# Kernel tuning notes

Measured on AMD Instinct MI355X. Metric: run time of the kernel, lower is better.

## Reference

```python
import math
import jax, jax.numpy as jnp
import numpy as np

B, L, HID = 2, 2048, 2048
H = 16
D = HID // H  # 128
EPS = 1e-6
ROPE_BASE = 10000.0
BETA_MIN, BETA_MAX = 0.8, 0.9995


def _rope_cache(seq_len, dim):
    half = dim // 2
    inv_freq = 1.0 / (ROPE_BASE ** (jnp.arange(half, dtype=jnp.float32) / float(half)))
    t = jnp.arange(seq_len, dtype=jnp.float32)
    freqs = t[:, None] * inv_freq[None, :]  # [L, half]
    return jnp.cos(freqs), jnp.sin(freqs)


def _apply_rope(x, cos, sin):
    # x: [B, H, L, D]; cos/sin: [L, D//2]
    half = x.shape[-1] // 2
    xe, xo = x[..., :half], x[..., half:]
    c = cos[None, None]
    s = sin[None, None]
    return jnp.concatenate([xe * c - xo * s, xe * s + xo * c], axis=-1)


def setup_inputs() -> dict:
    key = jax.random.key(0)
    ks = jax.random.split(key, 6)
    sc = 1.0 / math.sqrt(HID)  # ~ xavier scale
    return {
        "x": jax.random.normal(ks[0], (B, L, HID), jnp.float32),
        "Wq": jax.random.normal(ks[1], (HID, HID), jnp.float32) * sc,
        "Wk": jax.random.normal(ks[2], (HID, HID), jnp.float32) * sc,
        "Wv": jax.random.normal(ks[3], (HID, HID), jnp.float32) * sc,
        "Wg": jax.random.normal(ks[4], (HID, H), jnp.float32) * sc,
        "bg": jnp.full((H,), math.log(0.98 / (1.0 - 0.98)), jnp.float32),
        "Wo": jax.random.normal(ks[5], (HID, HID), jnp.float32) * sc,
        "bo": jnp.zeros((HID,), jnp.float32),
    }


def _deltanet(x, Wq, Wk, Wv, Wg, bg, Wo, bo):
    Bb, Ll, _ = x.shape
    split = lambda t: t.reshape(Bb, Ll, H, D).transpose(0, 2, 1, 3)  # [B,H,L,D]
    q = split(x @ Wq)
    k = split(x @ Wk)
    v = split(x @ Wv)

    cos, sin = _rope_cache(Ll, D)
    q = _apply_rope(q, cos, sin)
    k = _apply_rope(k, cos, sin)

    beta = jax.nn.sigmoid(x @ Wg + bg)                # [B,L,H]
    beta = jnp.clip(beta, BETA_MIN, BETA_MAX).transpose(0, 2, 1)  # [B,H,L]

    phi_q = jax.nn.elu(q) + 1.0
    phi_k = jax.nn.elu(k) + 1.0

    # time-major for scan
    pq = phi_q.transpose(2, 0, 1, 3)  # [L,B,H,D]
    pk = phi_k.transpose(2, 0, 1, 3)
    vt = v.transpose(2, 0, 1, 3)
    bt = beta.transpose(2, 0, 1)      # [L,B,H]

    S0 = jnp.zeros((Bb, H, D, D), jnp.float32)
    z0 = jnp.zeros((Bb, H, D), jnp.float32)

    def step(carry, inp):
        S, z = carry
        pq_t, pk_t, v_t, b_t = inp
        S = S * b_t[..., None, None] + pk_t[..., :, None] * v_t[..., None, :]
        z = z * b_t[..., None] + pk_t
        numer = jnp.einsum('bhd,bhde->bhe', pq_t, S)
        denom = jnp.sum(pq_t * z, axis=-1, keepdims=True) + EPS
        return (S, z), numer / denom

    (_, _), y = jax.lax.scan(step, (S0, z0), (pq, pk, vt, bt))  # y: [L,B,H,D]
    y = y.transpose(1, 0, 2, 3).reshape(Bb, Ll, HID)  # [B,L,H*D]
    return y @ Wo + bo


def reference(x, Wq, Wk, Wv, Wg, bg, Wo, bo):
    return _deltanet(x, Wq, Wk, Wv, Wg, bg, Wo, bo)
```

## Files before the change

kernel.cpp:

```cpp
#include <hip/hip_runtime.h>


typedef __attribute__((ext_vector_type(8))) short short8;
typedef __attribute__((ext_vector_type(4))) float f32x4;

__device__ __forceinline__ unsigned short f2bf(float f) {
  unsigned u = __float_as_uint(f);
  u += 0x7fffu + ((u >> 16) & 1u);
  return (unsigned short)(u >> 16);
}
__device__ __forceinline__ float bf2f(unsigned short s) {
  return __uint_as_float(((unsigned)s) << 16);
}
__device__ __forceinline__ float phi_elu1(float x) {
  return x > 0.f ? x + 1.f : expf(x);
}
__device__ __forceinline__ void gl_lds16(const void* g, void* l) {
  __builtin_amdgcn_global_load_lds(
      (const __attribute__((address_space(1))) void*)g,
      (__attribute__((address_space(3))) void*)l, 16, 0, 0);
}
__device__ __forceinline__ void bar_raw() {
  asm volatile("" ::: "memory");
  __builtin_amdgcn_s_barrier();
  asm volatile("" ::: "memory");
}

__global__ __launch_bounds__(256)
void k_cast(const float* __restrict__ x, unsigned short* __restrict__ xb) {
  int i = (blockIdx.x * 256 + threadIdx.x) * 4;
  float4 f = *(const float4*)(x + i);
  uint2 p;
  p.x = (unsigned)f2bf(f.x) | ((unsigned)f2bf(f.y) << 16);
  p.y = (unsigned)f2bf(f.z) | ((unsigned)f2bf(f.w) << 16);
  *(uint2*)(xb + i) = p;
}

__global__ __launch_bounds__(256)
void k_transw(const float* __restrict__ Wq, const float* __restrict__ Wk,
              const float* __restrict__ Wv, const float* __restrict__ Wo,
              const float* __restrict__ Wg,
              unsigned short* __restrict__ Wt, unsigned short* __restrict__ Wot,
              unsigned short* __restrict__ Wgt16) {
  const int z = blockIdx.z;
  if (z == 4) {
    if (blockIdx.y != 0) return;
    int idx = blockIdx.x * 256 + threadIdx.x;
    int h = idx >> 9, k4 = (idx & 511) * 4;
    uint2 p;
    p.x = (unsigned)f2bf(Wg[(k4 + 0) * 16 + h]) | ((unsigned)f2bf(Wg[(k4 + 1) * 16 + h]) << 16);
    p.y = (unsigned)f2bf(Wg[(k4 + 2) * 16 + h]) | ((unsigned)f2bf(Wg[(k4 + 3) * 16 + h]) << 16);
    *(uint2*)(Wgt16 + (size_t)h * 2048 + k4) = p;
    return;
  }
  const float* W = (z == 0) ? Wq : (z == 1) ? Wk : (z == 2) ? Wv : Wo;
  unsigned short* out = (z < 3) ? (Wt + (size_t)z * 2048 * 2048) : Wot;
  __shared__ float tile[64][65];
  const int n0 = blockIdx.x * 64;
  const int k0 = blockIdx.y * 64;
  const int tx = threadIdx.x & 63;
  const int ty = threadIdx.x >> 6;
#pragma unroll
  for (int rl = 0; rl < 16; ++rl) {
    int kk = rl * 4 + ty;
    tile[kk][tx] = W[(size_t)(k0 + kk) * 2048 + n0 + tx];
  }
  __syncthreads();
#pragma unroll
  for (int rl = 0; rl < 16; ++rl) {
    int nn = rl * 4 + ty;
    out[(size_t)(n0 + nn) * 2048 + k0 + tx] = f2bf(tile[tx][nn]);
  }
}

__global__ __launch_bounds__(256)
void k_betaW(const unsigned short* __restrict__ xb, const unsigned short* __restrict__ Wgt16,
             const float* __restrict__ bg, float* __restrict__ beta) {
  const int w = threadIdx.x >> 6;
  const int lane = threadIdx.x & 63;
  const int m = blockIdx.x * 4 + w;
  const int h = lane & 15, kq = lane >> 4;
  const unsigned short* xr = xb + (size_t)m * 2048 + kq * 512;
  const unsigned short* wr = Wgt16 + (size_t)h * 2048 + kq * 512;
  float acc = 0.f;
#pragma unroll 8
  for (int i = 0; i < 64; ++i) {
    short8 xv = *(const short8*)(xr + i * 8);
    short8 wv = *(const short8*)(wr + i * 8);
#pragma unroll
    for (int j = 0; j < 8; ++j)
      acc = fmaf(bf2f((unsigned short)xv[j]), bf2f((unsigned short)wv[j]), acc);
  }
  acc += __shfl_xor(acc, 16, 64);
  acc += __shfl_xor(acc, 32, 64);
  if (lane < 16) {
    float v = acc + bg[h];
    float bv = 1.f / (1.f + expf(-v));
    beta[(size_t)m * 16 + h] = fminf(fmaxf(bv, 0.8f), 0.9995f);
  }
}

template <bool OUT_BF16, bool ADD_BIAS>
__global__ __launch_bounds__(256)
void k_gemm(const unsigned short* __restrict__ A, const unsigned short* __restrict__ Bt,
            void* __restrict__ Cptr, const float* __restrict__ bias,
            int M, int N, int K, int ldA, int ldC) {
  __shared__ __align__(16) unsigned short As[128][64];
  __shared__ __align__(16) unsigned short Bs[128][64];
  const int tid = threadIdx.x;
  const int n0 = blockIdx.x * 128;
  const int m0 = blockIdx.y * 128;
  const int lane = tid & 63;
  const int w = tid >> 6;
  const int wm = w >> 1, wn = w & 1;
  const int q = lane >> 4, r = lane & 15;

  const int srow0 = w * 8 + (lane >> 3);
  const int scol = ((lane & 7) ^ ((lane >> 3) & 7)) * 8;

  f32x4 acc[4][4];
#pragma unroll
  for (int i = 0; i < 4; ++i)
#pragma unroll
    for (int j = 0; j < 4; ++j) acc[i][j] = (f32x4){0.f, 0.f, 0.f, 0.f};

  const unsigned short* A0 = A + (size_t)(m0 + srow0) * ldA + scol;
  const unsigned short* B0 = Bt + (size_t)(n0 + srow0) * K + scol;
  unsigned short* lA = &As[srow0][(lane & 7) * 8];
  unsigned short* lB = &Bs[srow0][(lane & 7) * 8];

  const int rsw = r & 7;

  for (int kt = 0; kt < K; kt += 64) {
    __syncthreads();
#pragma unroll
    for (int i = 0; i < 4; ++i) {
      gl_lds16(A0 + (size_t)i * 32 * ldA + kt, lA + i * 2048);
      gl_lds16(B0 + (size_t)i * 32 * K + kt, lB + i * 2048);
    }
    __syncthreads();
#pragma unroll
    for (int kk = 0; kk < 2; ++kk) {
      const int ps = ((kk * 4 + q) ^ rsw) * 8;
      short8 af[4], bfr[4];
#pragma unroll
      for (int i = 0; i < 4; ++i)
        af[i] = *(const short8*)&As[wm * 64 + i * 16 + r][ps];
#pragma unroll
      for (int j = 0; j < 4; ++j)
        bfr[j] = *(const short8*)&Bs[wn * 64 + j * 16 + r][ps];
#pragma unroll
      for (int i = 0; i < 4; ++i)
#pragma unroll
        for (int j = 0; j < 4; ++j)
          acc[i][j] = __builtin_amdgcn_mfma_f32_16x16x32_bf16(af[i], bfr[j], acc[i][j], 0, 0, 0);
    }
  }
#pragma unroll
  for (int i = 0; i < 4; ++i) {
#pragma unroll
    for (int j = 0; j < 4; ++j) {
#pragma unroll
      for (int rr = 0; rr < 4; ++rr) {
        int mi = m0 + wm * 64 + i * 16 + q * 4 + rr;
        int ni = n0 + wn * 64 + j * 16 + r;
        float val = acc[i][j][rr];
        if (ADD_BIAS) val += bias[ni];
        if (OUT_BF16)
          ((unsigned short*)Cptr)[(size_t)mi * ldC + ni] = f2bf(val);
        else
          ((float*)Cptr)[(size_t)mi * ldC + ni] = val;
      }
    }
  }
}

template <bool OUT_BF16, bool ADD_BIAS>
__global__ __launch_bounds__(512, 2)
void k_gemm2(const unsigned short* __restrict__ A, const unsigned short* __restrict__ Bt,
             void* __restrict__ Cptr, const float* __restrict__ bias,
             int M, int N, int K, int ldA, int ldC) {
  __shared__ __align__(16) unsigned short Ls[3][3][128][64];
  const int tid = threadIdx.x;
  const int lane = tid & 63;
  const int w = tid >> 6;
  const int wm = w >> 1;
  const int wn = w & 1;
  const int ql = lane >> 4;
  const int r = lane & 15;

  const int nwg = gridDim.x * gridDim.y;
  const int orig = blockIdx.y * gridDim.x + blockIdx.x;
  const int li = (orig & 7) * (nwg >> 3) + (orig >> 3);
  const int m0 = (li & 15) * 256;
  const int n0 = (li >> 4) * 128;

  const int srow = tid >> 3;
  const int sphys = tid & 7;
  const int slog = sphys ^ (srow & 7);
  const unsigned short* Ab = A + (size_t)(m0 + srow) * ldA + slog * 8;
  const unsigned short* Bb = Bt + (size_t)(n0 + srow) * K + slog * 8;

#define STG(st, h, tt)                                                        \
  do {                                                                        \
    const size_t ldx = ((h) == 2) ? (size_t)K : (size_t)ldA;                  \
    const unsigned short* gs =                                                \
        (((h) == 2) ? Bb : (Ab + (size_t)((h) * 128) * ldA)) +                \
        (size_t)(tt) * 64;                                                    \
    unsigned short* ld = &Ls[(st)][(h)][srow][sphys * 8];                     \
    gl_lds16(gs, ld);                                                         \
    gl_lds16(gs + 64 * ldx, ld + 64 * 64);                                    \
  } while (0)

  f32x4 acc[4][4];
#pragma unroll
  for (int i = 0; i < 4; ++i)
#pragma unroll
    for (int j = 0; j < 4; ++j) acc[i][j] = (f32x4){0.f, 0.f, 0.f, 0.f};

  const int NT = K >> 6;

#pragma unroll
  for (int h = 0; h < 3; ++h) STG(0, h, 0);
#pragma unroll
  for (int h = 0; h < 3; ++h) STG(1, h, 1);
  asm volatile("s_waitcnt vmcnt(6)" ::: "memory");
  bar_raw();

  short8 bfr[4][2];

  for (int t = 0; t < NT; ++t) {
    const int st = t % 3;
    const unsigned short (*LA)[64] = Ls[st][wm >> 1];
    const unsigned short (*LB)[64] = Ls[st][2];
    const int arow0 = (wm & 1) * 64;
    const int brow0 = wn * 64;
    const bool pf = (t + 2 < NT);
    const int s2 = (t + 2) % 3;
#pragma unroll
    for (int p = 0; p < 2; ++p) {
      if (p == 0) {
#pragma unroll
        for (int nj = 0; nj < 4; ++nj)
#pragma unroll
          for (int kk = 0; kk < 2; ++kk)
            bfr[nj][kk] = *(const short8*)
                &LB[brow0 + nj * 16 + r][((kk * 4 + ql) ^ (r & 7)) * 8];
      }
      short8 af[2][2];
#pragma unroll
      for (int im = 0; im < 2; ++im)
#pragma unroll
        for (int kk = 0; kk < 2; ++kk)
          af[im][kk] = *(const short8*)
              &LA[arow0 + (p * 2 + im) * 16 + r][((kk * 4 + ql) ^ (r & 7)) * 8];
      if (pf) {
        if (p == 0) {
          STG(s2, 0, t + 2);
          STG(s2, 1, t + 2);
        } else {
          STG(s2, 2, t + 2);
        }
      }
      bar_raw();
      __builtin_amdgcn_s_setprio(1);
#pragma unroll
      for (int kk = 0; kk < 2; ++kk)
#pragma unroll
        for (int im = 0; im < 2; ++im)
#pragma unroll
          for (int nj = 0; nj < 4; ++nj)
            acc[p * 2 + im][nj] = __builtin_amdgcn_mfma_f32_16x16x32_bf16(
                af[im][kk], bfr[nj][kk], acc[p * 2 + im][nj], 0, 0, 0);
      __builtin_amdgcn_s_setprio(0);
      if (p == 1) {
        if (pf)
          asm volatile("s_waitcnt vmcnt(6)" ::: "memory");
        else if (t + 1 < NT)
          asm volatile("s_waitcnt vmcnt(0)" ::: "memory");
      }
      __builtin_amdgcn_sched_barrier(0);
      bar_raw();
    }
  }
#undef STG

#pragma unroll
  for (int mi = 0; mi < 4; ++mi) {
#pragma unroll
    for (int nj = 0; nj < 4; ++nj) {
#pragma unroll
      for (int rr = 0; rr < 4; ++rr) {
        int mrow = m0 + wm * 64 + mi * 16 + ql * 4 + rr;
        int ncol = n0 + wn * 64 + nj * 16 + r;
        float val = acc[mi][nj][rr];
        if (ADD_BIAS) val += bias[ncol];
        if (OUT_BF16)
          ((unsigned short*)Cptr)[(size_t)mrow * ldC + ncol] = f2bf(val);
        else
          ((float*)Cptr)[(size_t)mrow * ldC + ncol] = val;
      }
    }
  }
}

__global__ __launch_bounds__(256)
void k_prep(const unsigned short* __restrict__ qkv, const float* __restrict__ beta,
            unsigned short* __restrict__ Qt, unsigned short* __restrict__ Ktg,
            unsigned short* __restrict__ Ag, unsigned short* __restrict__ Vg,
            float* __restrict__ gch) {
  const int ch = blockIdx.x;
  const int bh = blockIdx.y;
  const int b = bh >> 4, h = bh & 15;
  const int tid = threadIdx.x;
  const int t0 = ch * 64;

  __shared__ float Gs[64];
  __shared__ unsigned short Qs[64][136];
  __shared__ unsigned short Ks[64][136];
  __shared__ unsigned short Vs[128][72];

  if (tid < 64) {
    float bb = beta[((size_t)(b * 2048 + t0 + tid)) * 16 + h];
#pragma unroll
    for (int off = 1; off < 64; off <<= 1) {
      float o = __shfl_up(bb, off, 64);
      if (tid >= off) bb *= o;
    }
    Gs[tid] = bb;
    if (tid == 63) gch[bh * 32 + ch] = bb;
  }
  __syncthreads();

  const int dgl = tid & 7;
  float invf[8];
#pragma unroll
  for (int j = 0; j < 8; ++j)
    invf[j] = expf((float)(dgl * 8 + j) * -0.14391156831212787f);

  int s = tid >> 3;
#pragma unroll
  for (int rep = 0; rep < 2; ++rep, s += 32) {
    size_t row = ((size_t)(b * 2048 + t0 + s)) * 6144 + (size_t)h * 128;
    short8 qlo = *(const short8*)(qkv + row + dgl * 8);
    short8 qhi = *(const short8*)(qkv + row + 64 + dgl * 8);
    short8 klo = *(const short8*)(qkv + row + 2048 + dgl * 8);
    short8 khi = *(const short8*)(qkv + row + 2048 + 64 + dgl * 8);
    float g = Gs[s];
    float ig = 1.f / g;
    float tg = (float)(t0 + s);
    short8 oql, oqh, okl, okh;
#pragma unroll
    for (int j = 0; j < 8; ++j) {
      float sn, cs;
      __sincosf(tg * invf[j], &sn, &cs);
      float qe = bf2f((unsigned short)qlo[j]), qo = bf2f((unsigned short)qhi[j]);
      float a0 = qe * cs - qo * sn, a1 = qe * sn + qo * cs;
      oql[j] = (short)f2bf(phi_elu1(a0) * g);
      oqh[j] = (short)f2bf(phi_elu1(a1) * g);
      float ke = bf2f((unsigned short)klo[j]), ko = bf2f((unsigned short)khi[j]);
      a0 = ke * cs - ko * sn;
      a1 = ke * sn + ko * cs;
      okl[j] = (short)f2bf(phi_elu1(a0) * ig);
      okh[j] = (short)f2bf(phi_elu1(a1) * ig);
    }
    size_t qbase = (((size_t)bh * 32 + ch) * 64 + s) * 128;
    *(short8*)(Qt + qbase + dgl * 8) = oql;
    *(short8*)(Qt + qbase + 64 + dgl * 8) = oqh;
    *(short8*)&Qs[s][dgl * 8] = oql;
    *(short8*)&Qs[s][64 + dgl * 8] = oqh;
    *(short8*)&Ks[s][dgl * 8] = okl;
    *(short8*)&Ks[s][64 + dgl * 8] = okh;
  }
  {
    const int s2 = tid >> 2, qe = tid & 3;
    const unsigned short* vrow =
        qkv + ((size_t)(b * 2048 + t0 + s2)) * 6144 + 4096 + (size_t)h * 128 + qe * 32;
#pragma unroll
    for (int i = 0; i < 4; ++i) {
      short8 vv = *(const short8*)(vrow + i * 8);
#pragma unroll
      for (int j = 0; j < 8; ++j) Vs[qe * 32 + i * 8 + j][s2] = (unsigned short)vv[j];
    }
  }
  __syncthreads();

  {
    const int d = tid >> 1, sh = tid & 1;
    unsigned pk[16];
#pragma unroll
    for (int i = 0; i < 16; ++i)
      pk[i] = (unsigned)Ks[sh * 32 + 2 * i][d] | ((unsigned)Ks[sh * 32 + 2 * i + 1][d] << 16);
    unsigned short* kr = Ktg + ((size_t)bh * 32 + ch) * 8192 + (size_t)d * 64 + sh * 32;
#pragma unroll
    for (int i = 0; i < 4; ++i)
      *(uint4*)(kr + i * 8) = *(uint4*)&pk[i * 4];
    unsigned short* vr = Vg + ((size_t)bh * 32 + ch) * 8192 + (size_t)d * 64 + sh * 32;
#pragma unroll
    for (int i = 0; i < 4; ++i)
      *(uint4*)(vr + i * 8) = *(const uint4*)&Vs[d][sh * 32 + i * 8];
  }

  {
    const int lane = tid & 63;
    const int w = tid >> 6;
    const int q = lane >> 4, r = lane & 15;
    f32x4 acc[4];
#pragma unroll
    for (int nt = 0; nt < 4; ++nt) acc[nt] = (f32x4){0.f, 0.f, 0.f, 0.f};
#pragma unroll
    for (int kk = 0; kk < 4; ++kk) {
      short8 af = *(const short8*)&Qs[w * 16 + r][kk * 32 + q * 8];
#pragma unroll
      for (int nt = 0; nt < 4; ++nt) {
        short8 bf = *(const short8*)&Ks[nt * 16 + r][kk * 32 + q * 8];
        acc[nt] = __builtin_amdgcn_mfma_f32_16x16x32_bf16(af, bf, acc[nt], 0, 0, 0);
      }
    }
    unsigned short* Agp = Ag + ((size_t)bh * 32 + ch) * 4096;
#pragma unroll
    for (int nt = 0; nt < 4; ++nt) {
#pragma unroll
      for (int rr = 0; rr < 4; ++rr) {
        int t_l = w * 16 + q * 4 + rr;
        int s_l = nt * 16 + r;
        float val = (s_l <= t_l) ? acc[nt][rr] : 0.f;
        Agp[t_l * 64 + s_l] = f2bf(val);
      }
    }
  }
}

__global__ __launch_bounds__(256)
void k_kv(const unsigned short* __restrict__ Ktg, const unsigned short* __restrict__ Vg,
          unsigned short* __restrict__ Mg, float* __restrict__ mzg) {
  const int ch = blockIdx.x, bh = blockIdx.y;
  const int tid = threadIdx.x, lane = tid & 63, w = tid >> 6;
  const int q = lane >> 4, r = lane & 15;
  __shared__ unsigned short Kts[128][72];
  __shared__ unsigned short Vs[128][72];
  const unsigned short* Kp = Ktg + ((size_t)bh * 32 + ch) * 8192;
  const unsigned short* Vp = Vg + ((size_t)bh * 32 + ch) * 8192;
#pragma unroll
  for (int i = 0; i < 4; ++i) {
    int c = tid + i * 256;
    int dd = c >> 3, sg = c & 7;
    *(int4*)&Kts[dd][sg * 8] = *(const int4*)(Kp + dd * 64 + sg * 8);
    *(int4*)&Vs[dd][sg * 8] = *(const int4*)(Vp + dd * 64 + sg * 8);
  }
  __syncthreads();
  f32x4 acc[2][8];
#pragma unroll
  for (int jj = 0; jj < 2; ++jj)
#pragma unroll
    for (int i = 0; i < 8; ++i) acc[jj][i] = (f32x4){0.f, 0.f, 0.f, 0.f};
#pragma unroll
  for (int kk = 0; kk < 2; ++kk) {
    short8 af[2];
    af[0] = *(const short8*)&Vs[(w * 2 + 0) * 16 + r][kk * 32 + q * 8];
    af[1] = *(const short8*)&Vs[(w * 2 + 1) * 16 + r][kk * 32 + q * 8];
#pragma unroll
    for (int i = 0; i < 8; ++i) {
      short8 bf = *(const short8*)&Kts[i * 16 + r][kk * 32 + q * 8];
      acc[0][i] = __builtin_amdgcn_mfma_f32_16x16x32_bf16(af[0], bf, acc[0][i], 0, 0, 0);
      acc[1][i] = __builtin_amdgcn_mfma_f32_16x16x32_bf16(af[1], bf, acc[1][i], 0, 0, 0);
    }
  }
  {
    int dd = tid >> 1, sh = tid & 1;
    const unsigned short* kp = &Kts[dd][sh * 32];
    float zs = 0.f;
#pragma unroll
    for (int i = 0; i < 4; ++i) {
      short8 kv = *(const short8*)(kp + i * 8);
#pragma unroll
      for (int j = 0; j < 8; ++j) zs += bf2f((unsigned short)kv[j]);
    }
    zs += __shfl_xor(zs, 1, 64);
    if (sh == 0) mzg[((size_t)bh * 32 + ch) * 128 + dd] = zs;
  }
  unsigned short* Mp = Mg + ((size_t)bh * 32 + ch) * 16384;
#pragma unroll
  for (int jj = 0; jj < 2; ++jj)
#pragma unroll
    for (int i = 0; i < 8; ++i)
#pragma unroll
      for (int rr = 0; rr < 4; ++rr) {
        int e = (w * 2 + jj) * 16 + q * 4 + rr;
        Mp[e * 128 + i * 16 + r] = f2bf(acc[jj][i][rr]);
      }
}

__global__ __launch_bounds__(256)
void k_sprefix(unsigned short* __restrict__ Msg, float* __restrict__ mzg,
               const float* __restrict__ gch) {
  const int es = blockIdx.x;
  const int bh = blockIdx.y;
  const int tid = threadIdx.x;
  const int e = es * 16 + (tid >> 4);
  const int d0 = (tid & 15) * 8;
  unsigned short* base = Msg + (size_t)bh * 32 * 16384 + (size_t)e * 128 + d0;
  const float* gp = gch + bh * 32;
  float sv[8];
#pragma unroll
  for (int i = 0; i < 8; ++i) sv[i] = 0.f;
  uint4 mcur = *(const uint4*)base;
  for (int c = 0; c < 32; ++c) {
    uint4 mnext;
    if (c < 31) mnext = *(const uint4*)(base + (size_t)(c + 1) * 16384);
    uint4 so;
    so.x = (unsigned)f2bf(sv[0]) | ((unsigned)f2bf(sv[1]) << 16);
    so.y = (unsigned)f2bf(sv[2]) | ((unsigned)f2bf(sv[3]) << 16);
    so.z = (unsigned)f2bf(sv[4]) | ((unsigned)f2bf(sv[5]) << 16);
    so.w = (unsigned)f2bf(sv[6]) | ((unsigned)f2bf(sv[7]) << 16);
    *(uint4*)(base + (size_t)c * 16384) = so;
    float g = gp[c];
    const unsigned short* mp = (const unsigned short*)&mcur;
#pragma unroll
    for (int i = 0; i < 8; ++i) sv[i] = g * (sv[i] + bf2f(mp[i]));
    mcur = mnext;
  }
  if (es == 0 && tid < 128) {
    float* zb = mzg + (size_t)bh * 32 * 128 + tid;
    float z = 0.f;
    float zc = zb[0];
    for (int c = 0; c < 32; ++c) {
      float znext = (c < 31) ? zb[(size_t)(c + 1) * 128] : 0.f;
      zb[(size_t)c * 128] = z;
      z = gp[c] * (z + zc);
      zc = znext;
    }
  }
}

__global__ __launch_bounds__(256)
void k_out(const unsigned short* __restrict__ Qt, const unsigned short* __restrict__ Sg,
           const unsigned short* __restrict__ Ag, const unsigned short* __restrict__ Vg,
           const float* __restrict__ zg, unsigned short* __restrict__ numerb) {
  const int ch = blockIdx.x, bh = blockIdx.y;
  const int b = bh >> 4, h = bh & 15;
  const int tid = threadIdx.x, lane = tid & 63, w = tid >> 6;
  const int q = lane >> 4, r = lane & 15;
  __shared__ unsigned short Qs[64][136];
  __shared__ unsigned short Ss[128][136];
  __shared__ unsigned short As[64][72];
  __shared__ unsigned short Vs[128][72];
  __shared__ float zc[128];
  __shared__ float invs[64];

  const unsigned short* Qg = Qt + ((size_t)bh * 32 + ch) * 8192;
#pragma unroll
  for (int i = 0; i < 4; ++i) {
    int c = tid + i * 256;
    int ss = c >> 4, dg = c & 15;
    *(int4*)&Qs[ss][dg * 8] = *(const int4*)(Qg + ss * 128 + dg * 8);
  }
  const unsigned short* Sp = Sg + ((size_t)bh * 32 + ch) * 16384;
#pragma unroll
  for (int i = 0; i < 8; ++i) {
    int c = tid + i * 256;
    int e = c >> 4, dg = c & 15;
    *(int4*)&Ss[e][dg * 8] = *(const int4*)(Sp + e * 128 + dg * 8);
  }
#pragma unroll
  for (int i = 0; i < 2; ++i) {
    int c = tid + i * 256;
    int t_l = c >> 3, sg = c & 7;
    *(int4*)&As[t_l][sg * 8] =
        *(const int4*)(Ag + ((size_t)bh * 32 + ch) * 4096 + t_l * 64 + sg * 8);
  }
  const unsigned short* Vp = Vg + ((size_t)bh * 32 + ch) * 8192;
#pragma unroll
  for (int i = 0; i < 4; ++i) {
    int c = tid + i * 256;
    int e = c >> 3, sg = c & 7;
    *(int4*)&Vs[e][sg * 8] = *(const int4*)(Vp + e * 64 + sg * 8);
  }
  if (tid < 128) zc[tid] = zg[((size_t)bh * 32 + ch) * 128 + tid];
  __syncthreads();

  f32x4 nacc[8];
#pragma unroll
  for (int j = 0; j < 8; ++j) nacc[j] = (f32x4){0.f, 0.f, 0.f, 0.f};
#pragma unroll
  for (int kk = 0; kk < 4; ++kk) {
    short8 aq = *(const short8*)&Qs[w * 16 + r][kk * 32 + q * 8];
#pragma unroll
    for (int j = 0; j < 8; ++j) {
      short8 bf = *(const short8*)&Ss[j * 16 + r][kk * 32 + q * 8];
      nacc[j] = __builtin_amdgcn_mfma_f32_16x16x32_bf16(aq, bf, nacc[j], 0, 0, 0);
    }
  }
#pragma unroll
  for (int kk = 0; kk < 2; ++kk) {
    short8 aa = *(const short8*)&As[w * 16 + r][kk * 32 + q * 8];
#pragma unroll
    for (int j = 0; j < 8; ++j) {
      short8 bf = *(const short8*)&Vs[j * 16 + r][kk * 32 + q * 8];
      nacc[j] = __builtin_amdgcn_mfma_f32_16x16x32_bf16(aa, bf, nacc[j], 0, 0, 0);
    }
  }
  {
    float dsum = 0.f;
#pragma unroll
    for (int kk = 0; kk < 4; ++kk) {
      short8 aq = *(const short8*)&Qs[w * 16 + r][kk * 32 + q * 8];
      const float* zp = &zc[kk * 32 + q * 8];
      float4 z0a = *(const float4*)zp;
      float4 z0b = *(const float4*)(zp + 4);
      dsum = fmaf(bf2f((unsigned short)aq[0]), z0a.x, dsum);
      dsum = fmaf(bf2f((unsigned short)aq[1]), z0a.y, dsum);
      dsum = fmaf(bf2f((unsigned short)aq[2]), z0a.z, dsum);
      dsum = fmaf(bf2f((unsigned short)aq[3]), z0a.w, dsum);
      dsum = fmaf(bf2f((unsigned short)aq[4]), z0b.x, dsum);
      dsum = fmaf(bf2f((unsigned short)aq[5]), z0b.y, dsum);
      dsum = fmaf(bf2f((unsigned short)aq[6]), z0b.z, dsum);
      dsum = fmaf(bf2f((unsigned short)aq[7]), z0b.w, dsum);
    }
#pragma unroll
    for (int kk = 0; kk < 2; ++kk) {
      short8 aa = *(const short8*)&As[w * 16 + r][kk * 32 + q * 8];
#pragma unroll
      for (int j = 0; j < 8; ++j) dsum += bf2f((unsigned short)aa[j]);
    }
    dsum += __shfl_xor(dsum, 16, 64);
    dsum += __shfl_xor(dsum, 32, 64);
    if (lane < 16) invs[w * 16 + lane] = 1.f / (dsum + 1e-6f);
  }
  __syncthreads();
#pragma unroll
  for (int j = 0; j < 8; ++j) {
#pragma unroll
    for (int rr = 0; rr < 4; ++rr) {
      int t_l = w * 16 + q * 4 + rr;
      size_t m = (size_t)b * 2048 + ch * 64 + t_l;
      numerb[m * 2048 + h * 128 + j * 16 + r] = f2bf(nacc[j][rr] * invs[t_l]);
    }
  }
}

extern "C" void kernel_launch(void* const* d_in, const int* in_sizes, int n_in,
                              void* d_out, int out_size, void* d_ws, size_t ws_size,
                              hipStream_t stream) {
  const float* x  = (const float*)d_in[0];
  const float* Wq = (const float*)d_in[1];
  const float* Wk = (const float*)d_in[2];
  const float* Wv = (const float*)d_in[3];
  const float* Wg = (const float*)d_in[4];
  const float* bg = (const float*)d_in[5];
  const float* Wo = (const float*)d_in[6];
  const float* bo = (const float*)d_in[7];

  char* ws = (char*)d_ws;
  unsigned short* xb    = (unsigned short*)(ws);
  unsigned short* Qt    = (unsigned short*)(ws);
  unsigned short* Wt    = (unsigned short*)(ws + 16777216);
  unsigned short* Ktg   = (unsigned short*)(ws + 16777216);
  unsigned short* Ag    = (unsigned short*)(ws + 33554432);
  unsigned short* Wot   = (unsigned short*)(ws + 41943040);
  unsigned short* qkvb  = (unsigned short*)(ws + 50331648);
  unsigned short* Mg    = (unsigned short*)(ws + 50331648);
  float*          mzg   = (float*)(ws + 83886080);
  unsigned short* numerb= (unsigned short*)(ws + 100663296);
  unsigned short* Vg    = (unsigned short*)(ws + 117440512);
  float*          beta  = (float*)(ws + 134217728);
  unsigned short* Wgt16 = (unsigned short*)(ws + 134479872);
  float*          gch   = (float*)d_out;

  k_cast<<<8192, 256, 0, stream>>>(x, xb);
  k_transw<<<dim3(32, 32, 5), 256, 0, stream>>>(Wq, Wk, Wv, Wo, Wg, Wt, Wot, Wgt16);
  k_gemm<true, false><<<dim3(48, 32), 256, 0, stream>>>(
      xb, Wt, qkvb, nullptr, 4096, 6144, 2048, 2048, 6144);
  k_betaW<<<1024, 256, 0, stream>>>(xb, Wgt16, bg, beta);
  k_prep<<<dim3(32, 32), 256, 0, stream>>>(qkvb, beta, Qt, Ktg, Ag, Vg, gch);
  k_kv<<<dim3(32, 32), 256, 0, stream>>>(Ktg, Vg, Mg, mzg);
  k_sprefix<<<dim3(8, 32), 256, 0, stream>>>(Mg, mzg, gch);
  k_out<<<dim3(32, 32), 256, 0, stream>>>(Qt, Mg, Ag, Vg, mzg, numerb);
  k_gemm2<false, true><<<dim3(16, 16), 512, 0, stream>>>(
      numerb, Wot, d_out, bo, 4096, 2048, 2048, 2048, 2048);
}
```

Before: 407.0 us.

## Fuse chunk KV-state computation into prep kernel and swizzle GEMM tiles

The separate k_kv kernel is folded into k_prep: the transposed K tile stays in shared memory and the per-chunk V^T K state and key sums are computed right there, so the Ktg round trip through global memory and one launch go away. Both GEMMs get a grouped block-index remap to improve L2 reuse, the prefix-scan loads are batched four chunks at a time, and the LDS row padding shrinks. Buffers are relocated, with Mg now staged in the output buffer. The prep kernel uses more shared memory and registers, which may lower its occupancy.

```diff
diff --git a/kernel.cpp b/kernel.cpp
--- a/kernel.cpp
+++ b/kernel.cpp
@@ -108,8 +108,11 @@
   __shared__ __align__(16) unsigned short As[128][64];
   __shared__ __align__(16) unsigned short Bs[128][64];
   const int tid = threadIdx.x;
-  const int n0 = blockIdx.x * 128;
-  const int m0 = blockIdx.y * 128;
+  const int nwg = gridDim.x * gridDim.y;
+  const int orig = blockIdx.y * gridDim.x + blockIdx.x;
+  const int li = (orig & 7) * (nwg >> 3) + (orig >> 3);
+  const int n0 = (li % gridDim.x) * 128;
+  const int m0 = (li / gridDim.x) * 128;
   const int lane = tid & 63;
   const int w = tid >> 6;
   const int wm = w >> 1, wn = w & 1;
@@ -192,8 +195,8 @@
   const int nwg = gridDim.x * gridDim.y;
   const int orig = blockIdx.y * gridDim.x + blockIdx.x;
   const int li = (orig & 7) * (nwg >> 3) + (orig >> 3);
-  const int m0 = (li & 15) * 256;
-  const int n0 = (li >> 4) * 128;
+  const int m0 = (li >> 4) * 256;
+  const int n0 = (li & 15) * 128;
 
   const int srow = tid >> 3;
   const int sphys = tid & 7;
@@ -306,9 +309,9 @@
 
 __global__ __launch_bounds__(256)
 void k_prep(const unsigned short* __restrict__ qkv, const float* __restrict__ beta,
-            unsigned short* __restrict__ Qt, unsigned short* __restrict__ Ktg,
-            unsigned short* __restrict__ Ag, unsigned short* __restrict__ Vg,
-            float* __restrict__ gch) {
+            unsigned short* __restrict__ Qt, unsigned short* __restrict__ Ag,
+            unsigned short* __restrict__ Vg, unsigned short* __restrict__ Mg,
+            float* __restrict__ mzg, float* __restrict__ gch) {
   const int ch = blockIdx.x;
   const int bh = blockIdx.y;
   const int b = bh >> 4, h = bh & 15;
@@ -316,9 +319,10 @@
   const int t0 = ch * 64;
 
   __shared__ float Gs[64];
-  __shared__ unsigned short Qs[64][136];
-  __shared__ unsigned short Ks[64][136];
+  __shared__ unsigned short Qs[64][132];
+  __shared__ unsigned short Ks[64][132];
   __shared__ unsigned short Vs[128][72];
+  __shared__ unsigned short Kts[128][72];
 
   if (tid < 64) {
     float bb = beta[((size_t)(b * 2048 + t0 + tid)) * 16 + h];
@@ -391,10 +395,17 @@
 #pragma unroll
     for (int i = 0; i < 16; ++i)
       pk[i] = (unsigned)Ks[sh * 32 + 2 * i][d] | ((unsigned)Ks[sh * 32 + 2 * i + 1][d] << 16);
-    unsigned short* kr = Ktg + ((size_t)bh * 32 + ch) * 8192 + (size_t)d * 64 + sh * 32;
 #pragma unroll
     for (int i = 0; i < 4; ++i)
-      *(uint4*)(kr + i * 8) = *(uint4*)&pk[i * 4];
+      *(uint4*)&Kts[d][sh * 32 + i * 8] = *(uint4*)&pk[i * 4];
+    float zs = 0.f;
+#pragma unroll
+    for (int i = 0; i < 16; ++i) {
+      zs += bf2f((unsigned short)(pk[i] & 0xffffu));
+      zs += bf2f((unsigned short)(pk[i] >> 16));
+    }
+    zs += __shfl_xor(zs, 1, 64);
+    if (sh == 0) mzg[((size_t)bh * 32 + ch) * 128 + d] = zs;
     unsigned short* vr = Vg + ((size_t)bh * 32 + ch) * 8192 + (size_t)d * 64 + sh * 32;
 #pragma unroll
     for (int i = 0; i < 4; ++i)
@@ -429,66 +440,41 @@
       }
     }
   }
-}
-
-__global__ __launch_bounds__(256)
-void k_kv(const unsigned short* __restrict__ Ktg, const unsigned short* __restrict__ Vg,
-          unsigned short* __restrict__ Mg, float* __restrict__ mzg) {
-  const int ch = blockIdx.x, bh = blockIdx.y;
-  const int tid = threadIdx.x, lane = tid & 63, w = tid >> 6;
-  const int q = lane >> 4, r = lane & 15;
-  __shared__ unsigned short Kts[128][72];
-  __shared__ unsigned short Vs[128][72];
-  const unsigned short* Kp = Ktg + ((size_t)bh * 32 + ch) * 8192;
-  const unsigned short* Vp = Vg + ((size_t)bh * 32 + ch) * 8192;
-#pragma unroll
-  for (int i = 0; i < 4; ++i) {
-    int c = tid + i * 256;
-    int dd = c >> 3, sg = c & 7;
-    *(int4*)&Kts[dd][sg * 8] = *(const int4*)(Kp + dd * 64 + sg * 8);
-    *(int4*)&Vs[dd][sg * 8] = *(const int4*)(Vp + dd * 64 + sg * 8);
-  }
+
   __syncthreads();
-  f32x4 acc[2][8];
-#pragma unroll
-  for (int jj = 0; jj < 2; ++jj)
-#pragma unroll
-    for (int i = 0; i < 8; ++i) acc[jj][i] = (f32x4){0.f, 0.f, 0.f, 0.f};
-#pragma unroll
-  for (int kk = 0; kk < 2; ++kk) {
-    short8 af[2];
-    af[0] = *(const short8*)&Vs[(w * 2 + 0) * 16 + r][kk * 32 + q * 8];
-    af[1] = *(const short8*)&Vs[(w * 2 + 1) * 16 + r][kk * 32 + q * 8];
-#pragma unroll
-    for (int i = 0; i < 8; ++i) {
-      short8 bf = *(const short8*)&Kts[i * 16 + r][kk * 32 + q * 8];
-      acc[0][i] = __builtin_amdgcn_mfma_f32_16x16x32_bf16(af[0], bf, acc[0][i], 0, 0, 0);
-      acc[1][i] = __builtin_amdgcn_mfma_f32_16x16x32_bf16(af[1], bf, acc[1][i], 0, 0, 0);
-    }
-  }
+
   {
-    int dd = tid >> 1, sh = tid & 1;
-    const unsigned short* kp = &Kts[dd][sh * 32];
-    float zs = 0.f;
-#pragma unroll
-    for (int i = 0; i < 4; ++i) {
-      short8 kv = *(const short8*)(kp + i * 8);
-#pragma unroll
-      for (int j = 0; j < 8; ++j) zs += bf2f((unsigned short)kv[j]);
-    }
-    zs += __shfl_xor(zs, 1, 64);
-    if (sh == 0) mzg[((size_t)bh * 32 + ch) * 128 + dd] = zs;
-  }
-  unsigned short* Mp = Mg + ((size_t)bh * 32 + ch) * 16384;
-#pragma unroll
-  for (int jj = 0; jj < 2; ++jj)
-#pragma unroll
-    for (int i = 0; i < 8; ++i)
-#pragma unroll
-      for (int rr = 0; rr < 4; ++rr) {
-        int e = (w * 2 + jj) * 16 + q * 4 + rr;
-        Mp[e * 128 + i * 16 + r] = f2bf(acc[jj][i][rr]);
-      }
+    const int lane = tid & 63;
+    const int w = tid >> 6;
+    const int q = lane >> 4, r = lane & 15;
+    f32x4 acc[2][8];
+#pragma unroll
+    for (int jj = 0; jj < 2; ++jj)
+#pragma unroll
+      for (int i = 0; i < 8; ++i) acc[jj][i] = (f32x4){0.f, 0.f, 0.f, 0.f};
+#pragma unroll
+    for (int kk = 0; kk < 2; ++kk) {
+      short8 af[2];
+      af[0] = *(const short8*)&Vs[(w * 2 + 0) * 16 + r][kk * 32 + q * 8];
+      af[1] = *(const short8*)&Vs[(w * 2 + 1) * 16 + r][kk * 32 + q * 8];
+#pragma unroll
+      for (int i = 0; i < 8; ++i) {
+        short8 bf = *(const short8*)&Kts[i * 16 + r][kk * 32 + q * 8];
+        acc[0][i] = __builtin_amdgcn_mfma_f32_16x16x32_bf16(af[0], bf, acc[0][i], 0, 0, 0);
+        acc[1][i] = __builtin_amdgcn_mfma_f32_16x16x32_bf16(af[1], bf, acc[1][i], 0, 0, 0);
+      }
+    }
+    unsigned short* Mp = Mg + ((size_t)bh * 32 + ch) * 16384;
+#pragma unroll
+    for (int jj = 0; jj < 2; ++jj)
+#pragma unroll
+      for (int i = 0; i < 8; ++i)
+#pragma unroll
+        for (int rr = 0; rr < 4; ++rr) {
+          int e = (w * 2 + jj) * 16 + q * 4 + rr;
+          Mp[e * 128 + i * 16 + r] = f2bf(acc[jj][i][rr]);
+        }
+  }
 }
 
 __global__ __launch_bounds__(256)
@@ -504,31 +490,50 @@
   float sv[8];
 #pragma unroll
   for (int i = 0; i < 8; ++i) sv[i] = 0.f;
-  uint4 mcur = *(const uint4*)base;
-  for (int c = 0; c < 32; ++c) {
-    uint4 mnext;
-    if (c < 31) mnext = *(const uint4*)(base + (size_t)(c + 1) * 16384);
-    uint4 so;
-    so.x = (unsigned)f2bf(sv[0]) | ((unsigned)f2bf(sv[1]) << 16);
-    so.y = (unsigned)f2bf(sv[2]) | ((unsigned)f2bf(sv[3]) << 16);
-    so.z = (unsigned)f2bf(sv[4]) | ((unsigned)f2bf(sv[5]) << 16);
-    so.w = (unsigned)f2bf(sv[6]) | ((unsigned)f2bf(sv[7]) << 16);
-    *(uint4*)(base + (size_t)c * 16384) = so;
-    float g = gp[c];
-    const unsigned short* mp = (const unsigned short*)&mcur;
-#pragma unroll
-    for (int i = 0; i < 8; ++i) sv[i] = g * (sv[i] + bf2f(mp[i]));
-    mcur = mnext;
+  uint4 mb[2][4];
+#pragma unroll
+  for (int i = 0; i < 4; ++i) mb[0][i] = *(const uint4*)(base + (size_t)i * 16384);
+#pragma unroll
+  for (int g = 0; g < 8; ++g) {
+    if (g < 7) {
+#pragma unroll
+      for (int i = 0; i < 4; ++i)
+        mb[(g + 1) & 1][i] = *(const uint4*)(base + (size_t)(4 * (g + 1) + i) * 16384);
+    }
+#pragma unroll
+    for (int i = 0; i < 4; ++i) {
+      const int c = 4 * g + i;
+      uint4 so;
+      so.x = (unsigned)f2bf(sv[0]) | ((unsigned)f2bf(sv[1]) << 16);
+      so.y = (unsigned)f2bf(sv[2]) | ((unsigned)f2bf(sv[3]) << 16);
+      so.z = (unsigned)f2bf(sv[4]) | ((unsigned)f2bf(sv[5]) << 16);
+      so.w = (unsigned)f2bf(sv[6]) | ((unsigned)f2bf(sv[7]) << 16);
+      *(uint4*)(base + (size_t)c * 16384) = so;
+      float gv = gp[c];
+      const unsigned short* mp = (const unsigned short*)&mb[g & 1][i];
+#pragma unroll
+      for (int j = 0; j < 8; ++j) sv[j] = gv * (sv[j] + bf2f(mp[j]));
+    }
   }
   if (es == 0 && tid < 128) {
     float* zb = mzg + (size_t)bh * 32 * 128 + tid;
     float z = 0.f;
-    float zc = zb[0];
-    for (int c = 0; c < 32; ++c) {
-      float znext = (c < 31) ? zb[(size_t)(c + 1) * 128] : 0.f;
-      zb[(size_t)c * 128] = z;
-      z = gp[c] * (z + zc);
-      zc = znext;
+    float zv[2][4];
+#pragma unroll
+    for (int i = 0; i < 4; ++i) zv[0][i] = zb[(size_t)i * 128];
+#pragma unroll
+    for (int g = 0; g < 8; ++g) {
+      if (g < 7) {
+#pragma unroll
+        for (int i = 0; i < 4; ++i)
+          zv[(g + 1) & 1][i] = zb[(size_t)(4 * (g + 1) + i) * 128];
+      }
+#pragma unroll
+      for (int i = 0; i < 4; ++i) {
+        const int c = 4 * g + i;
+        zb[(size_t)c * 128] = z;
+        z = gp[c] * (z + zv[g & 1][i]);
+      }
     }
   }
 }
@@ -541,8 +546,8 @@
   const int b = bh >> 4, h = bh & 15;
   const int tid = threadIdx.x, lane = tid & 63, w = tid >> 6;
   const int q = lane >> 4, r = lane & 15;
-  __shared__ unsigned short Qs[64][136];
-  __shared__ unsigned short Ss[128][136];
+  __shared__ unsigned short Qs[64][132];
+  __shared__ unsigned short Ss[128][132];
   __shared__ unsigned short As[64][72];
   __shared__ unsigned short Vs[128][72];
   __shared__ float zc[128];
@@ -655,25 +660,23 @@
   unsigned short* xb    = (unsigned short*)(ws);
   unsigned short* Qt    = (unsigned short*)(ws);
   unsigned short* Wt    = (unsigned short*)(ws + 16777216);
-  unsigned short* Ktg   = (unsigned short*)(ws + 16777216);
+  float*          mzg   = (float*)(ws + 16777216);
+  float*          gch   = (float*)(ws + 17301504);
   unsigned short* Ag    = (unsigned short*)(ws + 33554432);
   unsigned short* Wot   = (unsigned short*)(ws + 41943040);
   unsigned short* qkvb  = (unsigned short*)(ws + 50331648);
-  unsigned short* Mg    = (unsigned short*)(ws + 50331648);
-  float*          mzg   = (float*)(ws + 83886080);
   unsigned short* numerb= (unsigned short*)(ws + 100663296);
   unsigned short* Vg    = (unsigned short*)(ws + 117440512);
   float*          beta  = (float*)(ws + 134217728);
   unsigned short* Wgt16 = (unsigned short*)(ws + 134479872);
-  float*          gch   = (float*)d_out;
+  unsigned short* Mg    = (unsigned short*)d_out;
 
   k_cast<<<8192, 256, 0, stream>>>(x, xb);
   k_transw<<<dim3(32, 32, 5), 256, 0, stream>>>(Wq, Wk, Wv, Wo, Wg, Wt, Wot, Wgt16);
   k_gemm<true, false><<<dim3(48, 32), 256, 0, stream>>>(
       xb, Wt, qkvb, nullptr, 4096, 6144, 2048, 2048, 6144);
   k_betaW<<<1024, 256, 0, stream>>>(xb, Wgt16, bg, beta);
-  k_prep<<<dim3(32, 32), 256, 0, stream>>>(qkvb, beta, Qt, Ktg, Ag, Vg, gch);
-  k_kv<<<dim3(32, 32), 256, 0, stream>>>(Ktg, Vg, Mg, mzg);
+  k_prep<<<dim3(32, 32), 256, 0, stream>>>(qkvb, beta, Qt, Ag, Vg, Mg, mzg, gch);
   k_sprefix<<<dim3(8, 32), 256, 0, stream>>>(Mg, mzg, gch);
   k_out<<<dim3(32, 32), 256, 0, stream>>>(Qt, Mg, Ag, Vg, mzg, numerb);
   k_gemm2<false, true><<<dim3(16, 16), 512, 0, stream>>>(
```

Measured after the change: 410.1 us. About the same (+0.8%).
